# Kernel optimization log

Hardware: AMD Instinct MI355X
Metric: run time of the kernel (lower is better)

## Reference

```python
import jax, jax.numpy as jnp
import numpy as np

B, S, F = 2048, 64, 16
H = 512
E = 8
HORIZON = 8
HH = H // 2


def _lstm_cell(x, h, c, Wih, Whh, b):
    # PyTorch gate order: i, f, g, o
    z = x @ Wih.T + h @ Whh.T + b  # [B, 4H]
    i, f, g, o = jnp.split(z, 4, axis=-1)
    c2 = jax.nn.sigmoid(f) * c + jax.nn.sigmoid(i) * jnp.tanh(g)
    h2 = jax.nn.sigmoid(o) * jnp.tanh(c2)
    return h2, c2


def _run_lstm(xs, Wih, Whh, b):
    # xs: [S, B, in]; returns outs [S, B, H], h_n, c_n
    Bv = xs.shape[1]
    h0 = jnp.zeros((Bv, H), xs.dtype)
    c0 = jnp.zeros((Bv, H), xs.dtype)

    def step(carry, xt):
        h, c = carry
        h, c = _lstm_cell(xt, h, c, Wih, Whh, b)
        return (h, c), h

    (h_n, c_n), outs = jax.lax.scan(step, (h0, c0), xs)
    return outs, h_n, c_n


def setup_inputs() -> dict:
    key = jax.random.key(0)
    ks = iter(jax.random.split(key, 40))
    s = 1.0 / np.sqrt(H)

    def rn(shape, scale=None):
        sc = s if scale is None else scale
        return (jax.random.normal(next(ks), shape, dtype=jnp.float32) * sc)

    inp = {
        'x': jax.random.normal(next(ks), (B, S, F), dtype=jnp.float32),
        # encoder LSTM layer 0 (in=F) and layer 1 (in=H); b = b_ih + b_hh fused
        'enc_Wih0': rn((4 * H, F)), 'enc_Whh0': rn((4 * H, H)), 'enc_b0': rn((4 * H,)),
        'enc_Wih1': rn((4 * H, H)), 'enc_Whh1': rn((4 * H, H)), 'enc_b1': rn((4 * H,)),
        # decoder LSTM (in=4)
        'dec_Wih': rn((4 * H, 4)), 'dec_Whh': rn((4 * H, H)), 'dec_b': rn((4 * H,)),
        # gating MLP
        'gW1': rn((HH, H)), 'gb1': rn((HH,)), 'gW2': rn((E, HH)), 'gb2': rn((E,)),
        # experts, stacked over E: track(2), intensity(1), wind_abs(1)
        'tW1': rn((E, HH, H)), 'tb1': rn((E, HH)), 'tW2': rn((E, 2, HH)), 'tb2': rn((E, 2)),
        'iW1': rn((E, HH, H)), 'ib1': rn((E, HH)), 'iW2': rn((E, 1, HH)), 'ib2': rn((E, 1)),
        'wW1': rn((E, HH, H)), 'wb1': rn((E, HH)), 'wW2': rn((E, 1, HH)), 'wb2': rn((E, 1)),
    }
    return inp


def _forward(x, enc_Wih0, enc_Whh0, enc_b0, enc_Wih1, enc_Whh1, enc_b1,
             dec_Wih, dec_Whh, dec_b, gW1, gb1, gW2, gb2,
             tW1, tb1, tW2, tb2, iW1, ib1, iW2, ib2, wW1, wb1, wW2, wb2):
    xs = jnp.swapaxes(x, 0, 1)  # [S, B, F]
    outs0, _, _ = _run_lstm(xs, enc_Wih0, enc_Whh0, enc_b0)
    _, h_n, c_n = _run_lstm(outs0, enc_Wih1, enc_Whh1, enc_b1)
    # (attention-pooled context of encoder is computed then discarded in the
    #  original forward; it does not affect outputs, so it is omitted here)

    dec_in0 = jnp.zeros((x.shape[0], 4), x.dtype)

    def step(carry, _):
        h, c, dec_in = carry
        h, c = _lstm_cell(dec_in, h, c, dec_Wih, dec_Whh, dec_b)
        ctx = h  # [B, H]
        gates = jax.nn.softmax(jax.nn.relu(ctx @ gW1.T + gb1) @ gW2.T + gb2, axis=-1)  # [B, E]
        def expert(W1, b1, W2, b2):
            hdd = jax.nn.relu(jnp.einsum('ehd,bd->beh', W1, ctx) + b1)  # [B, E, HH]
            return jnp.einsum('eoh,beh->beo', W2, hdd) + b2  # [B, E, out]
        track_e = expert(tW1, tb1, tW2, tb2)   # [B, E, 2]
        dwind_e = expert(iW1, ib1, iW2, ib2)   # [B, E, 1]
        wind_e = expert(wW1, wb1, wW2, wb2)    # [B, E, 1]
        g = gates[:, :, None]
        track = (g * track_e).sum(1)  # [B, 2]
        dwind = (g * dwind_e).sum(1)  # [B, 1]
        wind = (g * wind_e).sum(1)    # [B, 1]
        dec_in2 = jnp.concatenate([track, dwind, wind], axis=-1)  # [B, 4]
        return (h, c, dec_in2), (track, dwind[:, 0], wind[:, 0], gates)

    _, (trk, dw, wa, gt) = jax.lax.scan(step, (h_n, c_n, dec_in0), None, length=HORIZON)
    # trk: [T, B, 2]; dw, wa: [T, B]; gt: [T, B, E]
    dlat = trk[:, :, 0].T  # [B, T]
    dlon = trk[:, :, 1].T
    track = jnp.concatenate([dlat, dlon], axis=1)  # [B, 2T]
    intensity = dw.T  # [B, T]
    wind_abs = wa.T   # [B, T]
    gates_avg = gt.mean(0)  # [B, E]
    return track, intensity, wind_abs, gates_avg


def reference(x, enc_Wih0, enc_Whh0, enc_b0, enc_Wih1, enc_Whh1, enc_b1,
              dec_Wih, dec_Whh, dec_b, gW1, gb1, gW2, gb2,
              tW1, tb1, tW2, tb2, iW1, ib1, iW2, ib2, wW1, wb1, wW2, wb2):
    return _forward(x, enc_Wih0, enc_Whh0, enc_b0, enc_Wih1, enc_Whh1, enc_b1,
                    dec_Wih, dec_Whh, dec_b, gW1, gb1, gW2, gb2,
                    tW1, tb1, tW2, tb2, iW1, ib1, iW2, ib2, wW1, wb1, wW2, wb2)
```

## Files before the change

kernel.cpp:

```cpp
#include <hip/hip_runtime.h>
#include <math.h>

#define B_SZ 2048
#define SEQ 64
#define H 512
#define G4 2048
#define HH 256
#define NE 8
#define HOR 8

typedef _Float16 v8h __attribute__((ext_vector_type(8)));
typedef _Float16 v4h __attribute__((ext_vector_type(4)));
typedef float v4f __attribute__((ext_vector_type(4)));

__device__ __forceinline__ void gld16(const void* g, void* l) {
    __builtin_amdgcn_global_load_lds((const __attribute__((address_space(1))) void*)g,
                                     (__attribute__((address_space(3))) void*)l, 16, 0, 0);
}
__device__ __forceinline__ v4f mfma16(v8h a, v8h b, v4f c) {
    return __builtin_amdgcn_mfma_f32_16x16x32_f16(a, b, c, 0, 0, 0);
}
__device__ __forceinline__ float rcp_(float x) { return __builtin_amdgcn_rcpf(x); }
__device__ __forceinline__ float sigf(float x) { return rcp_(1.f + __expf(-x)); }
__device__ __forceinline__ float tanhf_(float x) { return 1.f - 2.f * rcp_(1.f + __expf(2.f * x)); }


struct CellP {
    const _Float16* Af; int KTA;
    const _Float16* Bf;
    const float* bias; int KT;
    float* cst;
    _Float16* h1p; int h1kt, h1o;
    _Float16* h2p; int h2kt, h2o;
    const _Float16* xsrc; _Float16* xdst;
};

__global__ __launch_bounds__(256, 2)
void cell2_k(CellP P0, CellP P1, int zbase)
{
    __shared__ __align__(16) char smem[65536];
    const CellP& P = (blockIdx.z + zbase == 0) ? P0 : P1;
    _Float16* st = (_Float16*)smem;
    float* zb = (float*)smem;
    const int tid = threadIdx.x, lane = tid & 63, wv = tid >> 6;
    const int bx = blockIdx.x, by = blockIdx.y;
    const int NIT = P.KT >> 1;

    const _Float16* pA0 = P.Af + ((long)(by * 8 + 2 * wv) * P.KTA) * 512 + lane * 8;
    const _Float16* pA1 = P.Af + ((long)(by * 8 + 2 * wv + 1) * P.KTA) * 512 + lane * 8;
    const _Float16* pB0 = P.Bf + ((long)(bx * 8 + 2 * wv) * P.KT) * 512 + lane * 8;
    const _Float16* pB1 = P.Bf + ((long)(bx * 8 + 2 * wv + 1) * P.KT) * 512 + lane * 8;
    const int oA = 4 * wv * 512;
    const int oB = 8192 + 4 * wv * 512;
    const int wm = (wv & 1) * 64;
    const int fr = lane & 15, q4 = (lane >> 4) * 4;

    v4f acc[4][4];
    #pragma unroll
    for (int i = 0; i < 4; i++)
        #pragma unroll
        for (int j = 0; j < 4; j++) acc[i][j] = (v4f){0.f, 0.f, 0.f, 0.f};

    auto stage = [&](int buf, int it) {
        _Float16* d = st + buf * 16384;
        const long ko = (long)it * 1024;
        gld16(pA0 + ko,       d + oA);
        gld16(pA0 + ko + 512, d + oA + 512);
        gld16(pA1 + ko,       d + oA + 1024);
        gld16(pA1 + ko + 512, d + oA + 1536);
        gld16(pB0 + ko,       d + oB);
        gld16(pB0 + ko + 512, d + oB + 512);
        gld16(pB1 + ko,       d + oB + 1024);
        gld16(pB1 + ko + 512, d + oB + 1536);
    };

    stage(0, 0);
    for (int it = 0; it < NIT; ++it) {
        __syncthreads();
        if (it + 1 < NIT) stage((it & 1) ^ 1, it + 1);
        const _Float16* base = st + (it & 1) * 16384;
        #pragma unroll
        for (int p = 0; p < 2; ++p) {
            v8h bf[4];
            #pragma unroll
            for (int nt = 0; nt < 4; ++nt)
                bf[nt] = *(const v8h*)(base + 8192 + (((wv >> 1) * 4 + nt) * 2 + p) * 512 + lane * 8);
            #pragma unroll
            for (int mt = 0; mt < 4; ++mt) {
                v8h a = *(const v8h*)(base + (((wv & 1) * 4 + mt) * 2 + p) * 512 + lane * 8);
                #pragma unroll
                for (int nt = 0; nt < 4; ++nt)
                    acc[mt][nt] = mfma16(a, bf[nt], acc[mt][nt]);
            }
        }
    }

    #pragma unroll
    for (int half = 0; half < 2; ++half) {
        __syncthreads();
        if ((wv >> 1) == half) {
            #pragma unroll
            for (int mt = 0; mt < 4; ++mt)
                #pragma unroll
                for (int nt = 0; nt < 4; ++nt) {
                    int col = nt * 16 + fr;
                    float bv = P.bias[bx * 128 + half * 64 + col];
                    #pragma unroll
                    for (int r = 0; r < 4; ++r)
                        zb[(wm + mt * 16 + q4 + r) * 68 + col] = acc[mt][nt][r] + bv;
                }
        }
        __syncthreads();
        const int row = tid >> 1, u8 = (tid & 1) * 8;
        const long b = by * 128 + row;
        const int ug = bx * 32 + half * 16 + u8;
        float* cp = P.cst + b * 512 + ug;
        float4 cl0 = *(float4*)cp, cl1 = *(float4*)(cp + 4);
        float cv[8] = {cl0.x, cl0.y, cl0.z, cl0.w, cl1.x, cl1.y, cl1.z, cl1.w};
        v8h hv;
        #pragma unroll
        for (int i = 0; i < 8; ++i) {
            const float* zz = &zb[row * 68 + (u8 + i) * 4];
            float cn = sigf(zz[1]) * cv[i] + sigf(zz[0]) * tanhf_(zz[2]);
            cv[i] = cn;
            hv[i] = (_Float16)(sigf(zz[3]) * tanhf_(cn));
        }
        *(float4*)cp = make_float4(cv[0], cv[1], cv[2], cv[3]);
        *(float4*)(cp + 4) = make_float4(cv[4], cv[5], cv[6], cv[7]);
        {
            int kk = P.h1o + ug;
            long a = ((b >> 4) * (long)P.h1kt + (kk >> 5)) * 512 + (((kk & 31) >> 3) * 16 + (b & 15)) * 8;
            *(v8h*)(P.h1p + a) = hv;
        }
        if (P.h2p) {
            int kk = P.h2o + ug;
            long a = ((b >> 4) * (long)P.h2kt + (kk >> 5)) * 512 + (((kk & 31) >> 3) * 16 + (b & 15)) * 8;
            *(v8h*)(P.h2p + a) = hv;
        }
        if (half == 0 && P.xsrc != nullptr && bx == 0) {
            int mc = tid >> 5, l = tid & 31;
            v8h xv = *(const v8h*)(P.xsrc + ((long)(by * 8 + mc) * 32 + l) * 8);
            *(v8h*)(P.xdst + (((long)(by * 8 + mc)) * 18 + 16) * 512 + l * 8) = xv;
        }
    }
}

__global__ __launch_bounds__(256, 4)
void expert_k(const _Float16* __restrict__ Af, const _Float16* __restrict__ W1f,
              const float* __restrict__ b1, const float* __restrict__ w2all,
              float* __restrict__ pe, _Float16* __restrict__ t1)
{
    __shared__ __align__(16) char smem[32768];
    _Float16* st = (_Float16*)smem;
    float* red = (float*)smem;
    const int tid = threadIdx.x, lane = tid & 63, wv = tid >> 6;
    const int bx = blockIdx.x, by = blockIdx.y;
    const long z = blockIdx.z;

    const _Float16* pA0 = Af + ((long)(by * 8 + 2 * wv) * 18) * 512 + lane * 8;
    const _Float16* pA1 = Af + ((long)(by * 8 + 2 * wv + 1) * 18) * 512 + lane * 8;
    const _Float16* pB0 = W1f + ((z * 16 + bx * 8 + 2 * wv) * 16) * 512 + lane * 8;
    const _Float16* pB1 = W1f + ((z * 16 + bx * 8 + 2 * wv + 1) * 16) * 512 + lane * 8;
    const int oA0 = 2 * wv * 512, oA1 = oA0 + 512;
    const int oB0 = 4096 + 2 * wv * 512, oB1 = oB0 + 512;
    const int wm = (wv & 1) * 64, wn = (wv >> 1) * 64;
    const int fr = lane & 15, q4 = (lane >> 4) * 4;

    v4f acc[4][4];
    #pragma unroll
    for (int i = 0; i < 4; i++)
        #pragma unroll
        for (int j = 0; j < 4; j++) acc[i][j] = (v4f){0.f, 0.f, 0.f, 0.f};

    gld16(pA0, st + oA0); gld16(pA1, st + oA1);
    gld16(pB0, st + oB0); gld16(pB1, st + oB1);
    pA0 += 512; pA1 += 512; pB0 += 512; pB1 += 512;

    for (int kt = 0; kt < 16; ++kt) {
        __syncthreads();
        const int cur = kt & 1;
        if (kt + 1 < 16) {
            _Float16* nb = st + (cur ^ 1) * 8192;
            gld16(pA0, nb + oA0); gld16(pA1, nb + oA1);
            gld16(pB0, nb + oB0); gld16(pB1, nb + oB1);
            pA0 += 512; pA1 += 512; pB0 += 512; pB1 += 512;
        }
        const _Float16* base = st + cur * 8192;
        v8h bf[4];
        #pragma unroll
        for (int nt = 0; nt < 4; ++nt)
            bf[nt] = *(const v8h*)(base + 4096 + ((wv >> 1) * 4 + nt) * 512 + lane * 8);
        #pragma unroll
        for (int mt = 0; mt < 4; ++mt) {
            v8h a = *(const v8h*)(base + ((wv & 1) * 4 + mt) * 512 + lane * 8);
            #pragma unroll
            for (int nt = 0; nt < 4; ++nt)
                acc[mt][nt] = mfma16(a, bf[nt], acc[mt][nt]);
        }
    }
    __syncthreads();

    if (z == 24) {
        #pragma unroll
        for (int mt = 0; mt < 4; ++mt)
            #pragma unroll
            for (int nt = 0; nt < 4; ++nt) {
                int col = bx * 128 + wn + nt * 16 + fr;
                float bv = b1[24 * 256 + col];
                #pragma unroll
                for (int r = 0; r < 4; ++r) {
                    float v = fmaxf(acc[mt][nt][r] + bv, 0.f);
                    t1[(long)(by * 128 + wm + mt * 16 + q4 + r) * 256 + col] = (_Float16)v;
                }
            }
        return;
    }
    float w0[4], w1[4], bv[4];
    #pragma unroll
    for (int nt = 0; nt < 4; ++nt) {
        int col = bx * 128 + wn + nt * 16 + fr;
        w0[nt] = w2all[(z * 2 + 0) * 256 + col];
        w1[nt] = w2all[(z * 2 + 1) * 256 + col];
        bv[nt] = b1[z * 256 + col];
    }
    float p0[4][4], p1[4][4];
    #pragma unroll
    for (int mt = 0; mt < 4; ++mt)
        #pragma unroll
        for (int r = 0; r < 4; ++r) { p0[mt][r] = 0.f; p1[mt][r] = 0.f; }
    #pragma unroll
    for (int mt = 0; mt < 4; ++mt)
        #pragma unroll
        for (int nt = 0; nt < 4; ++nt)
            #pragma unroll
            for (int r = 0; r < 4; ++r) {
                float v = fmaxf(acc[mt][nt][r] + bv[nt], 0.f);
                p0[mt][r] = fmaf(v, w0[nt], p0[mt][r]);
                p1[mt][r] = fmaf(v, w1[nt], p1[mt][r]);
            }
    #pragma unroll
    for (int off = 1; off < 16; off <<= 1)
        #pragma unroll
        for (int mt = 0; mt < 4; ++mt)
            #pragma unroll
            for (int r = 0; r < 4; ++r) {
                p0[mt][r] += __shfl_xor(p0[mt][r], off, 64);
                p1[mt][r] += __shfl_xor(p1[mt][r], off, 64);
            }
    if ((lane & 15) == 0) {
        #pragma unroll
        for (int mt = 0; mt < 4; ++mt)
            #pragma unroll
            for (int r = 0; r < 4; ++r) {
                int rw = wm + mt * 16 + q4 + r;
                red[(((wv >> 1) * 128) + rw) * 2 + 0] = p0[mt][r];
                red[(((wv >> 1) * 128) + rw) * 2 + 1] = p1[mt][r];
            }
    }
    __syncthreads();
    if (tid < 128) {
        #pragma unroll
        for (int o = 0; o < 2; ++o) {
            float v = red[tid * 2 + o] + red[(128 + tid) * 2 + o];
            pe[(((long)bx * 24 + z) * 2 + o) * 2048 + by * 128 + tid] = v;
        }
    }
}

__global__ __launch_bounds__(256)
void fin_k(const _Float16* __restrict__ t1, const float* __restrict__ gW2,
           const float* __restrict__ gb2, const float* __restrict__ pe,
           const float* __restrict__ tb2, const float* __restrict__ ib2,
           const float* __restrict__ wb2,
           float* __restrict__ out, _Float16* __restrict__ dw, int step)
{
    const long b = blockIdx.x * 256 + threadIdx.x;
    float acc[NE];
    #pragma unroll
    for (int e = 0; e < NE; e++) acc[e] = gb2[e];
    for (int j = 0; j < 256; j += 8) {
        v8h tv = *(const v8h*)(t1 + b * 256 + j);
        #pragma unroll
        for (int k = 0; k < 8; ++k) {
            float xv = (float)tv[k];
            #pragma unroll
            for (int e = 0; e < NE; e++) acc[e] = fmaf(xv, gW2[e * 256 + j + k], acc[e]);
        }
    }
    float mx = -1e30f;
    #pragma unroll
    for (int e = 0; e < NE; e++) mx = fmaxf(mx, acc[e]);
    float s = 0.f;
    #pragma unroll
    for (int e = 0; e < NE; e++) { acc[e] = __expf(acc[e] - mx); s += acc[e]; }
    float inv = 1.f / s;
    float t0 = 0.f, t1v = 0.f, iv = 0.f, wvv = 0.f;
    #pragma unroll
    for (int e = 0; e < NE; e++) {
        float g = acc[e] * inv;
        float prev = step == 0 ? 0.f : out[32 * (long)B_SZ + b * NE + e];
        out[32 * (long)B_SZ + b * NE + e] = prev + g * (1.f / HOR);
        float s00 = pe[((0 * 24 + e) * 2 + 0) * 2048 + b] + pe[((1 * 24 + e) * 2 + 0) * 2048 + b];
        float s01 = pe[((0 * 24 + e) * 2 + 1) * 2048 + b] + pe[((1 * 24 + e) * 2 + 1) * 2048 + b];
        float s10 = pe[((0 * 24 + 8 + e) * 2 + 0) * 2048 + b] + pe[((1 * 24 + 8 + e) * 2 + 0) * 2048 + b];
        float s20 = pe[((0 * 24 + 16 + e) * 2 + 0) * 2048 + b] + pe[((1 * 24 + 16 + e) * 2 + 0) * 2048 + b];
        t0  += g * (s00 + tb2[e * 2 + 0]);
        t1v += g * (s01 + tb2[e * 2 + 1]);
        iv  += g * (s10 + ib2[e]);
        wvv += g * (s20 + wb2[e]);
    }
    out[b * 16 + step] = t0;
    out[b * 16 + 8 + step] = t1v;
    out[16 * (long)B_SZ + b * 8 + step] = iv;
    out[24 * (long)B_SZ + b * 8 + step] = wvv;
    v4h dv = {(_Float16)t0, (_Float16)t1v, (_Float16)iv, (_Float16)wvv};
    *(v4h*)(dw + ((b >> 4) * 18 + 16) * 512 + (b & 15) * 8) = dv;
}

__global__ __launch_bounds__(64)
void prep_wfrag(const float* __restrict__ s1, int K1, const float* __restrict__ s2, int K2,
                _Float16* __restrict__ dst, int KT,
                const float* __restrict__ bs, float* __restrict__ bd)
{
    const int nc = blockIdx.x, kt = blockIdx.y, l = threadIdx.x;
    const int nprime = nc * 16 + (l & 15);
    const int u = nprime >> 2, g = nprime & 3, srow = g * 512 + u;
    v8h v;
    #pragma unroll
    for (int j = 0; j < 8; ++j) {
        int k = kt * 32 + (l >> 4) * 8 + j;
        float val = 0.f;
        if (k < K1) val = s1[(long)srow * K1 + k];
        else if (k < K1 + K2) val = s2[(long)srow * K2 + k - K1];
        v[j] = (_Float16)val;
    }
    *(v8h*)(dst + ((long)nc * KT + kt) * 512 + l * 8) = v;
    if (kt == 0 && l < 16) bd[nc * 16 + l] = bs[((nc * 16 + l) & 3) * 512 + ((nc * 16 + l) >> 2)];
}

__global__ __launch_bounds__(64)
void prep_w1frag(const float* __restrict__ tW1, const float* __restrict__ iW1,
                 const float* __restrict__ wW1, const float* __restrict__ gW1,
                 _Float16* __restrict__ dst)
{
    const int nc = blockIdx.x & 15, kt = blockIdx.x >> 4, z = blockIdx.y, l = threadIdx.x;
    const float* src;
    if (z < 8) src = tW1 + (long)z * 256 * 512;
    else if (z < 16) src = iW1 + (long)(z - 8) * 256 * 512;
    else if (z < 24) src = wW1 + (long)(z - 16) * 256 * 512;
    else src = gW1;
    const int row = nc * 16 + (l & 15);
    v8h v;
    #pragma unroll
    for (int j = 0; j < 8; ++j)
        v[j] = (_Float16)src[(long)row * 512 + kt * 32 + (l >> 4) * 8 + j];
    *(v8h*)(dst + (((long)z * 16 + nc) * 16 + kt) * 512 + l * 8) = v;
}

__global__ __launch_bounds__(256)
void cat4(const float* __restrict__ a, const float* __restrict__ b,
          const float* __restrict__ c, const float* __restrict__ g,
          float* __restrict__ d)
{
    int i = blockIdx.x * 256 + threadIdx.x;
    float v;
    if (i < 2048) v = a[i];
    else if (i < 4096) v = b[i - 2048];
    else if (i < 6144) v = c[i - 4096];
    else v = g[i - 6144];
    d[i] = v;
}

__global__ __launch_bounds__(256)
void prep_w2(const float* __restrict__ tW2, const float* __restrict__ iW2,
             const float* __restrict__ wW2, float* __restrict__ W2all)
{
    int i = blockIdx.x * 256 + threadIdx.x;
    int j = i & 255, o = (i >> 8) & 1, zz = i >> 9;
    int br = zz >> 3, e = zz & 7;
    float v = 0.f;
    if (br == 0) v = tW2[(e * 2 + o) * 256 + j];
    else if (o == 0) v = (br == 1 ? iW2 : wW2)[e * 256 + j];
    W2all[i] = v;
}

__global__ __launch_bounds__(256)
void prep_xf(const float* __restrict__ x, _Float16* __restrict__ xTf,
             _Float16* __restrict__ act0a)
{
    const int t = blockIdx.x * 256 + threadIdx.x;
    const int l = t & 31, mc = (t >> 5) & 127, s = t >> 12;
    const long b = mc * 16 + (l & 15);
    const float* src = x + (b * 64 + s) * 16 + (l >> 4) * 8;
    v8h v;
    #pragma unroll
    for (int j = 0; j < 8; ++j) v[j] = (_Float16)src[j];
    *(v8h*)(xTf + (((long)s * 128 + mc) * 32 + l) * 8) = v;
    if (s == 0) *(v8h*)(act0a + ((long)mc * 18 + 16) * 512 + l * 8) = v;
}

extern "C" void kernel_launch(void* const* d_in, const int* in_sizes, int n_in,
                              void* d_out, int out_size, void* d_ws, size_t ws_size,
                              hipStream_t stream)
{
    const float* x    = (const float*)d_in[0];
    const float* Wih0 = (const float*)d_in[1];
    const float* Whh0 = (const float*)d_in[2];
    const float* b0   = (const float*)d_in[3];
    const float* Wih1 = (const float*)d_in[4];
    const float* Whh1 = (const float*)d_in[5];
    const float* b1   = (const float*)d_in[6];
    const float* dWih = (const float*)d_in[7];
    const float* dWhh = (const float*)d_in[8];
    const float* db   = (const float*)d_in[9];
    const float* gW1  = (const float*)d_in[10];
    const float* gb1  = (const float*)d_in[11];
    const float* gW2  = (const float*)d_in[12];
    const float* gb2  = (const float*)d_in[13];
    const float* tW1  = (const float*)d_in[14];
    const float* tb1  = (const float*)d_in[15];
    const float* tW2  = (const float*)d_in[16];
    const float* tb2  = (const float*)d_in[17];
    const float* iW1  = (const float*)d_in[18];
    const float* ib1  = (const float*)d_in[19];
    const float* iW2  = (const float*)d_in[20];
    const float* ib2  = (const float*)d_in[21];
    const float* wW1  = (const float*)d_in[22];
    const float* wb1  = (const float*)d_in[23];
    const float* wW2  = (const float*)d_in[24];
    const float* wb2  = (const float*)d_in[25];
    float* out = (float*)d_out;

    char* p = (char*)d_ws;
    auto alloc = [&](size_t bytes) { char* r = p; p += (bytes + 255) & ~255ULL; return r; };
    _Float16* xTf   = (_Float16*)alloc((size_t)SEQ * 128 * 32 * 8 * 2);
    _Float16* act0a = (_Float16*)alloc((size_t)128 * 18 * 512 * 2);
    _Float16* act0b = (_Float16*)alloc((size_t)128 * 18 * 512 * 2);
    _Float16* act1a = (_Float16*)alloc((size_t)128 * 32 * 512 * 2);
    _Float16* act1b = (_Float16*)alloc((size_t)128 * 32 * 512 * 2);
    _Float16* actDa = (_Float16*)alloc((size_t)128 * 18 * 512 * 2);
    _Float16* actDb = (_Float16*)alloc((size_t)128 * 18 * 512 * 2);
    float*    c0    = (float*)alloc((size_t)B_SZ * 512 * 4);
    float*    c1    = (float*)alloc((size_t)B_SZ * 512 * 4);
    _Float16* Wc0   = (_Float16*)alloc((size_t)128 * 18 * 512 * 2);
    _Float16* Wc1   = (_Float16*)alloc((size_t)128 * 32 * 512 * 2);
    _Float16* Wcd   = (_Float16*)alloc((size_t)128 * 18 * 512 * 2);
    float*    b0i   = (float*)alloc((size_t)G4 * 4);
    float*    b1i   = (float*)alloc((size_t)G4 * 4);
    float*    bdi   = (float*)alloc((size_t)G4 * 4);
    _Float16* W1all = (_Float16*)alloc((size_t)25 * 16 * 16 * 512 * 2);
    float*    b1all = (float*)alloc((size_t)25 * HH * 4);
    float*    W2all = (float*)alloc((size_t)24 * 2 * 256 * 4);
    _Float16* t1    = (_Float16*)alloc((size_t)B_SZ * HH * 2);
    float*    pe    = (float*)alloc((size_t)2 * 24 * 2 * 2048 * 4);

    hipMemsetAsync(act0a, 0, (size_t)128 * 18 * 512 * 2, stream);
    hipMemsetAsync(act0b, 0, (size_t)128 * 18 * 512 * 2, stream);
    hipMemsetAsync(act1a, 0, (size_t)128 * 32 * 512 * 2, stream);
    hipMemsetAsync(act1b, 0, (size_t)128 * 32 * 512 * 2, stream);
    hipMemsetAsync(actDa, 0, (size_t)128 * 18 * 512 * 2, stream);
    hipMemsetAsync(actDb, 0, (size_t)128 * 18 * 512 * 2, stream);
    hipMemsetAsync(c0, 0, (size_t)B_SZ * 512 * 4, stream);
    hipMemsetAsync(c1, 0, (size_t)B_SZ * 512 * 4, stream);

    prep_wfrag<<<dim3(128, 18), dim3(64), 0, stream>>>(Whh0, 512, Wih0, 16, Wc0, 18, b0, b0i);
    prep_wfrag<<<dim3(128, 32), dim3(64), 0, stream>>>(Wih1, 512, Whh1, 512, Wc1, 32, b1, b1i);
    prep_wfrag<<<dim3(128, 18), dim3(64), 0, stream>>>(dWhh, 512, dWih, 4, Wcd, 18, db, bdi);
    prep_w1frag<<<dim3(256, 25), dim3(64), 0, stream>>>(tW1, iW1, wW1, gW1, W1all);
    cat4<<<dim3(25), dim3(256), 0, stream>>>(tb1, ib1, wb1, gb1, b1all);
    prep_w2<<<dim3(48), dim3(256), 0, stream>>>(tW2, iW2, wW2, W2all);
    prep_xf<<<dim3(1024), dim3(256), 0, stream>>>(x, xTf, act0a);

    _Float16* act0[2] = {act0a, act0b};
    _Float16* act1[2] = {act1a, act1b};

    for (int s = 0; s <= SEQ; ++s) {
        const bool do0 = (s < SEQ), do1 = (s >= 1);
        CellP P0 = {}, P1 = {};
        if (do0) {
            P0.Af = act0[s & 1]; P0.KTA = 18;
            P0.Bf = Wc0; P0.bias = b0i; P0.KT = 18;
            P0.cst = c0;
            P0.h1p = act0[(s + 1) & 1]; P0.h1kt = 18; P0.h1o = 0;
            P0.h2p = act1[s & 1]; P0.h2kt = 32; P0.h2o = 0;
            P0.xsrc = (s < SEQ - 1) ? (xTf + ((long)(s + 1) * 128 * 32) * 8) : nullptr;
            P0.xdst = act0[(s + 1) & 1];
        }
        if (do1) {
            P1.Af = act1[(s + 1) & 1]; P1.KTA = 32;
            P1.Bf = Wc1; P1.bias = b1i; P1.KT = 32;
            P1.cst = c1;
            P1.h1p = act1[s & 1]; P1.h1kt = 32; P1.h1o = 512;
            P1.h2p = (s == SEQ) ? actDa : nullptr; P1.h2kt = 18; P1.h2o = 0;
            P1.xsrc = nullptr; P1.xdst = nullptr;
        }
        const int nz = (do0 && do1) ? 2 : 1;
        const int zbase = do0 ? 0 : 1;
        cell2_k<<<dim3(16, 16, nz), dim3(256), 0, stream>>>(P0, P1, zbase);
    }

    for (int t = 0; t < HOR; ++t) {
        _Float16* dr = (t & 1) ? actDb : actDa;
        _Float16* dw = (t & 1) ? actDa : actDb;
        CellP PD = {};
        PD.Af = dr; PD.KTA = 18;
        PD.Bf = Wcd; PD.bias = bdi; PD.KT = 18;
        PD.cst = c1;
        PD.h1p = dw; PD.h1kt = 18; PD.h1o = 0;
        PD.h2p = nullptr; PD.xsrc = nullptr; PD.xdst = nullptr;
        cell2_k<<<dim3(16, 16, 1), dim3(256), 0, stream>>>(PD, PD, 0);
        expert_k<<<dim3(2, 16, 25), dim3(256), 0, stream>>>(dw, W1all, b1all, W2all, pe, t1);
        fin_k<<<dim3(8), dim3(256), 0, stream>>>(t1, gW2, gb2, pe, tb2, ib2, wb2, out, dw, t);
    }
}
```

Baseline: 1.952 ms.

## Shrink LSTM cell GEMM tile to 64x128 with 2-wave blocks and single-k stages

Changes the fused LSTM cell kernel from 256-thread blocks computing a 128x128 tile to 128-thread blocks computing a 64x128 tile. Each k-step now stages one 32-wide slice instead of two, and LDS drops from 64KB to about 34KB. The grid doubles along batch to 512 or 1024 blocks, which should fill more CUs on the latency-bound per-timestep launches. The epilogue is reorganised so each thread handles 16 units. In exchange, the B operand (weights) is reused across fewer rows per block, so global and L2 weight traffic rises.

```diff
diff --git a/kernel.cpp b/kernel.cpp
--- a/kernel.cpp
+++ b/kernel.cpp
@@ -35,24 +35,24 @@
     const _Float16* xsrc; _Float16* xdst;
 };
 
-__global__ __launch_bounds__(256, 2)
+__global__ __launch_bounds__(128, 2)
 void cell2_k(CellP P0, CellP P1, int zbase)
 {
-    __shared__ __align__(16) char smem[65536];
+    __shared__ __align__(16) char smem[34816];
     const CellP& P = (blockIdx.z + zbase == 0) ? P0 : P1;
     _Float16* st = (_Float16*)smem;
     float* zb = (float*)smem;
     const int tid = threadIdx.x, lane = tid & 63, wv = tid >> 6;
     const int bx = blockIdx.x, by = blockIdx.y;
-    const int NIT = P.KT >> 1;
-
-    const _Float16* pA0 = P.Af + ((long)(by * 8 + 2 * wv) * P.KTA) * 512 + lane * 8;
-    const _Float16* pA1 = P.Af + ((long)(by * 8 + 2 * wv + 1) * P.KTA) * 512 + lane * 8;
-    const _Float16* pB0 = P.Bf + ((long)(bx * 8 + 2 * wv) * P.KT) * 512 + lane * 8;
-    const _Float16* pB1 = P.Bf + ((long)(bx * 8 + 2 * wv + 1) * P.KT) * 512 + lane * 8;
-    const int oA = 4 * wv * 512;
-    const int oB = 8192 + 4 * wv * 512;
-    const int wm = (wv & 1) * 64;
+    const int KT = P.KT;
+
+    const _Float16* src[6];
+    #pragma unroll
+    for (int e = 0; e < 6; ++e) {
+        int g = wv * 6 + e;
+        if (g < 4) src[e] = P.Af + ((long)(by * 4 + g) * P.KTA) * 512 + lane * 8;
+        else       src[e] = P.Bf + ((long)(bx * 8 + (g - 4)) * KT) * 512 + lane * 8;
+    }
     const int fr = lane & 15, q4 = (lane >> 4) * 4;
 
     v4f acc[4][4];
@@ -61,86 +61,80 @@
         #pragma unroll
         for (int j = 0; j < 4; j++) acc[i][j] = (v4f){0.f, 0.f, 0.f, 0.f};
 
-    auto stage = [&](int buf, int it) {
-        _Float16* d = st + buf * 16384;
-        const long ko = (long)it * 1024;
-        gld16(pA0 + ko,       d + oA);
-        gld16(pA0 + ko + 512, d + oA + 512);
-        gld16(pA1 + ko,       d + oA + 1024);
-        gld16(pA1 + ko + 512, d + oA + 1536);
-        gld16(pB0 + ko,       d + oB);
-        gld16(pB0 + ko + 512, d + oB + 512);
-        gld16(pB1 + ko,       d + oB + 1024);
-        gld16(pB1 + ko + 512, d + oB + 1536);
+    auto stage = [&](int buf) {
+        _Float16* d = st + buf * 6144;
+        #pragma unroll
+        for (int e = 0; e < 6; ++e) {
+            gld16(src[e], d + (wv * 6 + e) * 512);
+            src[e] += 512;
+        }
     };
 
-    stage(0, 0);
-    for (int it = 0; it < NIT; ++it) {
+    stage(0);
+    for (int kt = 0; kt < KT; ++kt) {
         __syncthreads();
-        if (it + 1 < NIT) stage((it & 1) ^ 1, it + 1);
-        const _Float16* base = st + (it & 1) * 16384;
-        #pragma unroll
-        for (int p = 0; p < 2; ++p) {
-            v8h bf[4];
+        if (kt + 1 < KT) stage((kt & 1) ^ 1);
+        const _Float16* base = st + (kt & 1) * 6144;
+        v8h bf[4];
+        #pragma unroll
+        for (int nt = 0; nt < 4; ++nt)
+            bf[nt] = *(const v8h*)(base + (4 + wv * 4 + nt) * 512 + lane * 8);
+        #pragma unroll
+        for (int mt = 0; mt < 4; ++mt) {
+            v8h a = *(const v8h*)(base + mt * 512 + lane * 8);
             #pragma unroll
             for (int nt = 0; nt < 4; ++nt)
-                bf[nt] = *(const v8h*)(base + 8192 + (((wv >> 1) * 4 + nt) * 2 + p) * 512 + lane * 8);
-            #pragma unroll
-            for (int mt = 0; mt < 4; ++mt) {
-                v8h a = *(const v8h*)(base + (((wv & 1) * 4 + mt) * 2 + p) * 512 + lane * 8);
-                #pragma unroll
-                for (int nt = 0; nt < 4; ++nt)
-                    acc[mt][nt] = mfma16(a, bf[nt], acc[mt][nt]);
-            }
-        }
-    }
-
-    #pragma unroll
-    for (int half = 0; half < 2; ++half) {
-        __syncthreads();
-        if ((wv >> 1) == half) {
-            #pragma unroll
-            for (int mt = 0; mt < 4; ++mt)
-                #pragma unroll
-                for (int nt = 0; nt < 4; ++nt) {
-                    int col = nt * 16 + fr;
-                    float bv = P.bias[bx * 128 + half * 64 + col];
-                    #pragma unroll
-                    for (int r = 0; r < 4; ++r)
-                        zb[(wm + mt * 16 + q4 + r) * 68 + col] = acc[mt][nt][r] + bv;
-                }
-        }
-        __syncthreads();
-        const int row = tid >> 1, u8 = (tid & 1) * 8;
-        const long b = by * 128 + row;
-        const int ug = bx * 32 + half * 16 + u8;
-        float* cp = P.cst + b * 512 + ug;
-        float4 cl0 = *(float4*)cp, cl1 = *(float4*)(cp + 4);
-        float cv[8] = {cl0.x, cl0.y, cl0.z, cl0.w, cl1.x, cl1.y, cl1.z, cl1.w};
-        v8h hv;
-        #pragma unroll
-        for (int i = 0; i < 8; ++i) {
-            const float* zz = &zb[row * 68 + (u8 + i) * 4];
+                acc[mt][nt] = mfma16(a, bf[nt], acc[mt][nt]);
+        }
+    }
+
+    __syncthreads();
+    #pragma unroll
+    for (int mt = 0; mt < 4; ++mt)
+        #pragma unroll
+        for (int nt = 0; nt < 4; ++nt) {
+            int col = wv * 64 + nt * 16 + fr;
+            float bv = P.bias[bx * 128 + col];
+            #pragma unroll
+            for (int r = 0; r < 4; ++r)
+                zb[(mt * 16 + q4 + r) * 132 + col] = acc[mt][nt][r] + bv;
+        }
+    __syncthreads();
+    {
+        const int row = tid >> 1, u16 = (tid & 1) * 16;
+        const long b = (long)by * 64 + row;
+        float* cp = P.cst + b * 512 + bx * 32 + u16;
+        float cv[16] __attribute__((aligned(16)));
+        #pragma unroll
+        for (int q = 0; q < 4; ++q) *(float4*)&cv[q * 4] = *(const float4*)(cp + q * 4);
+        v8h hv[2];
+        #pragma unroll
+        for (int i = 0; i < 16; ++i) {
+            const float* zz = &zb[row * 132 + (u16 + i) * 4];
             float cn = sigf(zz[1]) * cv[i] + sigf(zz[0]) * tanhf_(zz[2]);
             cv[i] = cn;
-            hv[i] = (_Float16)(sigf(zz[3]) * tanhf_(cn));
-        }
-        *(float4*)cp = make_float4(cv[0], cv[1], cv[2], cv[3]);
-        *(float4*)(cp + 4) = make_float4(cv[4], cv[5], cv[6], cv[7]);
-        {
-            int kk = P.h1o + ug;
+            hv[i >> 3][i & 7] = (_Float16)(sigf(zz[3]) * tanhf_(cn));
+        }
+        #pragma unroll
+        for (int q = 0; q < 4; ++q) *(float4*)(cp + q * 4) = *(const float4*)&cv[q * 4];
+        #pragma unroll
+        for (int half = 0; half < 2; ++half) {
+            int kk = P.h1o + bx * 32 + u16 + half * 8;
             long a = ((b >> 4) * (long)P.h1kt + (kk >> 5)) * 512 + (((kk & 31) >> 3) * 16 + (b & 15)) * 8;
-            *(v8h*)(P.h1p + a) = hv;
+            *(v8h*)(P.h1p + a) = hv[half];
         }
         if (P.h2p) {
-            int kk = P.h2o + ug;
-            long a = ((b >> 4) * (long)P.h2kt + (kk >> 5)) * 512 + (((kk & 31) >> 3) * 16 + (b & 15)) * 8;
-            *(v8h*)(P.h2p + a) = hv;
-        }
-        if (half == 0 && P.xsrc != nullptr && bx == 0) {
-            int mc = tid >> 5, l = tid & 31;
-            v8h xv = *(const v8h*)(P.xsrc + ((long)(by * 8 + mc) * 32 + l) * 8);
-            *(v8h*)(P.xdst + (((long)(by * 8 + mc)) * 18 + 16) * 512 + l * 8) = xv;
+            #pragma unroll
+            for (int half = 0; half < 2; ++half) {
+                int kk = P.h2o + bx * 32 + u16 + half * 8;
+                long a = ((b >> 4) * (long)P.h2kt + (kk >> 5)) * 512 + (((kk & 31) >> 3) * 16 + (b & 15)) * 8;
+                *(v8h*)(P.h2p + a) = hv[half];
+            }
+        }
+        if (P.xsrc != nullptr && bx == 0) {
+            int mc = by * 4 + (tid >> 5), l = tid & 31;
+            v8h xv = *(const v8h*)(P.xsrc + ((long)mc * 32 + l) * 8);
+            *(v8h*)(P.xdst + ((long)mc * 18 + 16) * 512 + l * 8) = xv;
         }
     }
 }
@@ -496,7 +490,7 @@
         }
         const int nz = (do0 && do1) ? 2 : 1;
         const int zbase = do0 ? 0 : 1;
-        cell2_k<<<dim3(16, 16, nz), dim3(256), 0, stream>>>(P0, P1, zbase);
+        cell2_k<<<dim3(16, 32, nz), dim3(128), 0, stream>>>(P0, P1, zbase);
     }
 
     for (int t = 0; t < HOR; ++t) {
@@ -508,7 +502,7 @@
         PD.cst = c1;
         PD.h1p = dw; PD.h1kt = 18; PD.h1o = 0;
         PD.h2p = nullptr; PD.xsrc = nullptr; PD.xdst = nullptr;
-        cell2_k<<<dim3(16, 16, 1), dim3(256), 0, stream>>>(PD, PD, 0);
+        cell2_k<<<dim3(16, 32, 1), dim3(128), 0, stream>>>(PD, PD, 0);
         expert_k<<<dim3(2, 16, 25), dim3(256), 0, stream>>>(dw, W1all, b1all, W2all, pe, t1);
         fin_k<<<dim3(8), dim3(256), 0, stream>>>(t1, gW2, gb2, pe, tb2, ib2, wb2, out, dw, t);
     }
```

After: 2.125 ms. +8.9%, slower.
